# Kernel tuning notes

Measured on AMD Instinct MI355X. Metric: run time of the kernel, lower is better.

The kernel has to match this reference:

```python
import jax, jax.numpy as jnp
import numpy as np

NUM_EMBEDDINGS = 1024
EMBEDDING_DIM = 256
COMMITMENT_COST = 0.02


def setup_inputs() -> dict:
    key = jax.random.key(0)
    k1, k2 = jax.random.split(key)
    z = jax.random.normal(k1, (64, 256, 32, 32), dtype=jnp.float32)
    # torch init: uniform(-1/K, 1/K)
    emb = jax.random.uniform(k2, (NUM_EMBEDDINGS, EMBEDDING_DIM), dtype=jnp.float32,
                             minval=-1.0 / NUM_EMBEDDINGS, maxval=1.0 / NUM_EMBEDDINGS)
    return {"z": z, "emb": emb}


def reference(z, emb):
    n, d, h, w = z.shape
    # (N, D, H, W) -> (N*H*W, D)
    z_flat = jnp.transpose(z, (0, 2, 3, 1)).reshape(-1, d)
    # squared L2 distances: ||z||^2 - 2 z.E^T + ||E||^2  -> (NHW, K)
    distances = (jnp.sum(z_flat * z_flat, axis=1, keepdims=True)
                 - 2.0 * z_flat @ emb.T
                 + jnp.sum(emb * emb, axis=1))
    indices = jnp.argmin(distances, axis=1)  # (NHW,)
    z_q = jnp.transpose(emb[indices].reshape(n, h, w, d), (0, 3, 1, 2))  # (N, D, H, W)
    # straight-through estimator
    z_q_st = z + jax.lax.stop_gradient(z_q - z)
    commitment_loss = COMMITMENT_COST * jnp.mean((jax.lax.stop_gradient(z) - z_q) ** 2)
    codebook_loss = jnp.mean((z - jax.lax.stop_gradient(z_q)) ** 2)
    vq_loss = commitment_loss + codebook_loss
    indices_reshaped = indices.reshape(n, h, w)
    return z_q_st, indices_reshaped, vq_loss
```

## Files before the change

### kernel.cpp

```cpp
#include <hip/hip_runtime.h>
#include <hip/hip_bf16.h>
#include <float.h>

#define OUT_IDX_OFF 16777216
#define OUT_LOSS_OFF 16842752
#define CAND_OFF 8388608
#define GMIN_OFF 12582912
#define GCNT_OFF 13107200
#define NSLOT 32
#define DELTA 2.0e-3f

typedef __attribute__((ext_vector_type(8))) short short8;
typedef __attribute__((ext_vector_type(4))) float f32x4;

static __device__ __forceinline__ unsigned short f2bf(float f) {
  union { __hip_bfloat16 h; unsigned short u; } cv;
  cv.h = __float2bfloat16(f);
  return cv.u;
}

__global__ __launch_bounds__(256) void k_prep(const float* __restrict__ emb,
                                              unsigned short* __restrict__ E2,
                                              float* __restrict__ cws,
                                              int* __restrict__ gmin,
                                              int* __restrict__ gcnt,
                                              float* __restrict__ out) {
  const int k = blockIdx.x, d = threadIdx.x;
  const int tid = (k << 8) + d;
  if (tid < 65536) {
    gmin[tid] = 0x7f7f7f7f;
    gcnt[tid] = 0;
  }
  if (tid == 0) out[OUT_LOSS_OFF] = 0.0f;
  const float v = emb[k * 256 + d];
  __shared__ float red[256];
  __shared__ unsigned short row[256];
  row[d] = f2bf(v);
  red[d] = v * v;
  __syncthreads();
  for (int s = 128; s > 0; s >>= 1) {
    if (d < s) red[d] += red[d + s];
    __syncthreads();
  }
  if (d == 0) cws[k] = red[0];
  if (d < 32) ((short8*)&E2[k * 256])[d] = ((short8*)row)[d];
}

__global__ __launch_bounds__(256) void k_cvt4(const float* __restrict__ z,
                                              unsigned short* __restrict__ A2,
                                              float* __restrict__ aws) {
#pragma clang fp contract(off)
  __shared__ float tile[64][65];
  __shared__ float red2[128];
  const int t = threadIdx.x;
  const int p0 = blockIdx.x << 6;
  const int n = p0 >> 10, hw0 = p0 & 1023;
  const float* zb = z + (size_t)n * 262144 + hw0;
  const int hwl = (t & 15) << 2;
  const int dlb = t >> 4;
  const int row = t & 63, h = (t >> 6) & 1;
  const int pl = t >> 2, c = t & 3;

  float4 v[4];
#pragma unroll
  for (int i = 0; i < 4; ++i)
    v[i] = *(const float4*)&zb[(size_t)(dlb + i * 16) * 1024 + hwl];

  float acc[8];

  for (int dt = 0; dt < 4; ++dt) {
    if (dt) __syncthreads();
#pragma unroll
    for (int i = 0; i < 4; ++i) {
      const int dl = dlb + i * 16;
      tile[hwl + 0][dl] = v[i].x;
      tile[hwl + 1][dl] = v[i].y;
      tile[hwl + 2][dl] = v[i].z;
      tile[hwl + 3][dl] = v[i].w;
    }
    __syncthreads();
    if (dt < 3) {
      const float* zb2 = zb + (size_t)(dt + 1) * 65536;
#pragma unroll
      for (int i = 0; i < 4; ++i)
        v[i] = *(const float4*)&zb2[(size_t)(dlb + i * 16) * 1024 + hwl];
    }
    unsigned short* dst = &A2[(size_t)(p0 + pl) * 256 + dt * 64];
#pragma unroll
    for (int hh = 0; hh < 2; ++hh) {
      const int ch = c + hh * 4;
      unsigned short tmp[8];
#pragma unroll
      for (int j = 0; j < 8; ++j) tmp[j] = f2bf(tile[pl][ch * 8 + j]);
      *(short8*)&dst[ch * 8] = *(short8*)tmp;
    }
    if (t < 128 && (dt >> 1) == h) {
      if ((dt & 1) == 0) {
#pragma unroll
        for (int j = 0; j < 8; ++j) {
          const float x = tile[row][j];
          acc[j] = x * x;
        }
        for (int g = 1; g < 8; ++g)
#pragma unroll
          for (int j = 0; j < 8; ++j) {
            const float x = tile[row][g * 8 + j];
            const float p = x * x;
            acc[j] = acc[j] + p;
          }
      } else {
        for (int g = 8; g < 16; ++g)
#pragma unroll
          for (int j = 0; j < 8; ++j) {
            const float x = tile[row][(g - 8) * 8 + j];
            const float p = x * x;
            acc[j] = acc[j] + p;
          }
      }
    }
  }
  if (t < 128) {
    const float s = ((acc[0] + acc[1]) + (acc[2] + acc[3])) +
                    ((acc[4] + acc[5]) + (acc[6] + acc[7]));
    red2[t] = s;
  }
  __syncthreads();
  if (t < 64) aws[p0 + t] = red2[t] + red2[t + 64];
}

__global__ __launch_bounds__(256, 4) void k_gemm9(
    const unsigned short* __restrict__ A2, const unsigned short* __restrict__ E2,
    const float* __restrict__ cws, const float* __restrict__ aws,
    int* __restrict__ gmin, int* __restrict__ gcnt,
    float2* __restrict__ gcand) {
  __shared__ __align__(16) unsigned short As[128 * 64];
  __shared__ __align__(16) unsigned short Bs[128 * 64];
  __shared__ float a_l[128], c_l[128], rmkt[256], bmin[128];

  const int t = threadIdx.x;
  const int lane = t & 63;
  const int wave = __builtin_amdgcn_readfirstlane(t >> 6);
  const int wr = wave >> 1, wc = wave & 1;
  const int quad = lane >> 4, l15 = lane & 15;
  const int swa = l15 & 7;

  const int bid = blockIdx.x;
  const int L = ((bid & 7) << 9) + (bid >> 3);
  const int rb = L >> 3, ck = L & 7;
  const int r0 = rb << 7, k0 = ck << 7;

  if (t < 128) {
    a_l[t] = aws[r0 + t];
    c_l[t] = cws[k0 + t];
  }

  const int srow = t >> 3;
  const int gpos = t & 7;

  f32x4 acc[4][4];
#pragma unroll
  for (int a = 0; a < 4; ++a)
#pragma unroll
    for (int b = 0; b < 4; ++b) acc[a][b] = (f32x4)(0.0f);

  for (int kt = 0; kt < 4; ++kt) {
    if (kt) __syncthreads();
#pragma unroll
    for (int i = 0; i < 4; ++i) {
      const int row = (i << 5) + srow;
      const int gsrc = gpos ^ (row & 7);
      const unsigned short* sa =
          A2 + (((size_t)(r0 + row)) << 8) + (kt << 6) + (gsrc << 3);
      __builtin_amdgcn_global_load_lds(
          (const __attribute__((address_space(1))) void*)sa,
          (__attribute__((address_space(3))) void*)(As + (i << 11) +
                                                    (wave << 9)),
          16, 0, 0);
      const unsigned short* sb =
          E2 + (((size_t)(k0 + row)) << 8) + (kt << 6) + (gsrc << 3);
      __builtin_amdgcn_global_load_lds(
          (const __attribute__((address_space(1))) void*)sb,
          (__attribute__((address_space(3))) void*)(Bs + (i << 11) +
                                                    (wave << 9)),
          16, 0, 0);
    }
    __syncthreads();
#pragma unroll
    for (int ks = 0; ks < 2; ++ks) {
      short8 af[4], bf[4];
#pragma unroll
      for (int tr = 0; tr < 4; ++tr)
        af[tr] = *(const short8*)&As[(wr * 64 + tr * 16 + l15) * 64 +
                                     (((ks * 4 + quad) ^ swa) << 3)];
#pragma unroll
      for (int tc = 0; tc < 4; ++tc)
        bf[tc] = *(const short8*)&Bs[(wc * 64 + tc * 16 + l15) * 64 +
                                     (((ks * 4 + quad) ^ swa) << 3)];
#pragma unroll
      for (int tr = 0; tr < 4; ++tr)
#pragma unroll
        for (int tc = 0; tc < 4; ++tc)
          acc[tr][tc] = __builtin_amdgcn_mfma_f32_16x16x32_bf16(
              af[tr], bf[tc], acc[tr][tc], 0, 0, 0);
    }
  }

#pragma unroll
  for (int tr = 0; tr < 4; ++tr)
#pragma unroll
    for (int rg = 0; rg < 4; ++rg) {
      const int rloc = wr * 64 + tr * 16 + quad * 4 + rg;
      const float av = a_l[rloc];
      float mn = FLT_MAX;
#pragma unroll
      for (int tc = 0; tc < 4; ++tc) {
        const int cloc = wc * 64 + tc * 16 + l15;
        const float s = av + fmaf(-2.0f, acc[tr][tc][rg], c_l[cloc]);
        mn = fminf(mn, s);
      }
      mn = fminf(mn, __shfl_xor(mn, 1));
      mn = fminf(mn, __shfl_xor(mn, 2));
      mn = fminf(mn, __shfl_xor(mn, 4));
      mn = fminf(mn, __shfl_xor(mn, 8));
      if (l15 == 0) rmkt[rloc * 2 + wc] = mn;
    }
  __syncthreads();
  if (t < 128) {
    const float m = fminf(rmkt[t * 2], rmkt[t * 2 + 1]);
    const int old = atomicMin(&gmin[r0 + t], __float_as_int(m));
    bmin[t] = fminf(m, __int_as_float(old));
  }
  __syncthreads();
#pragma unroll
  for (int tr = 0; tr < 4; ++tr)
#pragma unroll
    for (int rg = 0; rg < 4; ++rg) {
      const int rloc = wr * 64 + tr * 16 + quad * 4 + rg;
      const float av = a_l[rloc];
      const float lim = bmin[rloc] + DELTA;
#pragma unroll
      for (int tc = 0; tc < 4; ++tc) {
        const int cloc = wc * 64 + tc * 16 + l15;
        const float s = av + fmaf(-2.0f, acc[tr][tc][rg], c_l[cloc]);
        if (s <= lim) {
          const int pos = atomicAdd(&gcnt[r0 + rloc], 1);
          if (pos < NSLOT)
            gcand[(size_t)(r0 + rloc) * NSLOT + pos] =
                make_float2(s, __int_as_float(k0 + cloc));
        }
      }
    }
}

__global__ __launch_bounds__(256) void k_finish6(
    const float* __restrict__ z, const float* __restrict__ emb,
    const float* __restrict__ cws, const float* __restrict__ aws,
    const int* __restrict__ gmin, const int* __restrict__ gcnt,
    const float2* __restrict__ gcand, int* __restrict__ idxws,
    float* __restrict__ out, int write_zq) {
  __shared__ float ztile[256][64];
  __shared__ int sidx[64];
  const int t = threadIdx.x;
  const int p0 = blockIdx.x << 6;
  const int n = p0 >> 10, hw0 = p0 & 1023;
  const float* zb = z + (size_t)n * 262144 + hw0;

  const int hwl = (t & 15) << 2;
  const int dl = t >> 4;
#pragma unroll
  for (int i = 0; i < 16; ++i) {
    const int d = dl + (i << 4);
    const float4 v = *(const float4*)&zb[(size_t)d * 1024 + hwl];
    ztile[d][hwl + 0] = v.x;
    ztile[d][hwl + 1] = v.y;
    ztile[d][hwl + 2] = v.z;
    ztile[d][hwl + 3] = v.w;
  }
  __syncthreads();

  const int pl = t >> 2, sub = t & 3;
  const int r = p0 + pl;
  const float lim = __int_as_float(gmin[r]) + DELTA;
  int m = gcnt[r];
  if (m > NSLOT) m = NSLOT;
  const float a = aws[r];
  float bestv = FLT_MAX;
  int besti = 0x7fffffff;
  for (int ci = sub; ci < m; ci += 4) {
    const float2 p = gcand[(size_t)r * NSLOT + ci];
    if (p.x > lim) continue;
    const int k = __float_as_int(p.y);
    const float4* ep4 = (const float4*)(emb + (size_t)k * 256);
    float dot = 0.0f;
#pragma unroll 16
    for (int j = 0; j < 64; ++j) {
      const float4 e = ep4[j];
      dot = fmaf(ztile[4 * j + 0][pl], e.x, dot);
      dot = fmaf(ztile[4 * j + 1][pl], e.y, dot);
      dot = fmaf(ztile[4 * j + 2][pl], e.z, dot);
      dot = fmaf(ztile[4 * j + 3][pl], e.w, dot);
    }
    float s = fmaf(-2.0f, dot, a);
    s = s + cws[k];
    if (s < bestv || (s == bestv && k < besti)) {
      bestv = s;
      besti = k;
    }
  }
#pragma unroll
  for (int off = 1; off < 4; off <<= 1) {
    const float ov = __shfl_xor(bestv, off);
    const int oi = __shfl_xor(besti, off);
    if (ov < bestv || (ov == bestv && oi < besti)) {
      bestv = ov;
      besti = oi;
    }
  }
  if (sub == 0) {
    out[OUT_IDX_OFF + r] = (float)besti;
    sidx[pl] = besti;
    if (!write_zq) idxws[r] = besti;
  }
  float c = (sub == 0) ? bestv : 0.0f;
#pragma unroll
  for (int off = 1; off < 64; off <<= 1) c += __shfl_xor(c, off);
  if ((t & 63) == 0)
    atomicAdd(&out[OUT_LOSS_OFF], c * (1.02f / 16777216.0f));

  if (write_zq) {
    __syncthreads();
    const int px = t & 63, dq = t >> 6;
    const float* ep = emb + (size_t)sidx[px] * 256 + (dq << 6);
    float* ob = out + (size_t)n * 262144 + ((size_t)(dq << 6)) * 1024 + hw0 + px;
#pragma unroll 8
    for (int i = 0; i < 64; ++i) ob[(size_t)i * 1024] = ep[i];
  }
}

__global__ __launch_bounds__(256) void k_out2(const float* __restrict__ emb,
                                              const int* __restrict__ idxws,
                                              float* __restrict__ out) {
  __shared__ float zq[32][257];
  __shared__ int sidx[32];
  const int t = threadIdx.x;
  const int p0 = blockIdx.x << 5;
  const int n = p0 >> 10, hw0 = p0 & 1023;
  if (t < 32) sidx[t] = idxws[p0 + t];
  __syncthreads();
#pragma unroll
  for (int it = 0; it < 8; ++it) {
    const int i = t + (it << 8);
    const int p = i >> 6;
    const int q = (i & 63) << 2;
    const float4 v = *(const float4*)&emb[(size_t)sidx[p] * 256 + q];
    zq[p][q] = v.x;
    zq[p][q + 1] = v.y;
    zq[p][q + 2] = v.z;
    zq[p][q + 3] = v.w;
  }
  __syncthreads();
  const int p = t & 31, d0 = t >> 5;
  float* ob = out + (size_t)n * 262144 + hw0 + p;
#pragma unroll
  for (int dd = 0; dd < 32; ++dd) {
    const int d = (dd << 3) + d0;
    ob[(size_t)d * 1024] = zq[p][d];
  }
}

extern "C" void kernel_launch(void* const* d_in, const int* in_sizes, int n_in,
                              void* d_out, int out_size, void* d_ws,
                              size_t ws_size, hipStream_t stream) {
  const float* z = (const float*)d_in[0];
  const float* emb = (const float*)d_in[1];
  float* out = (float*)d_out;

  unsigned short* E2 = (unsigned short*)d_ws;
  float* cws = (float*)(E2 + 262144);
  float* aws = cws + 1024;
  int* idxws = (int*)(aws + 65536);
  unsigned short* A2 = (unsigned short*)d_out;

  const size_t WS_NEED = 1052672u + 262144u + 262144u + 16777216u;
  const int big_ws = (ws_size >= WS_NEED) ? 1 : 0;
  int* gmin;
  int* gcnt;
  float2* gcand;
  if (big_ws) {
    gmin = idxws + 65536;
    gcnt = gmin + 65536;
    gcand = (float2*)(gcnt + 65536);
  } else {
    gcand = (float2*)(out + CAND_OFF);
    gmin = (int*)(out + GMIN_OFF);
    gcnt = (int*)(out + GCNT_OFF);
  }

  k_prep<<<dim3(1024), dim3(256), 0, stream>>>(emb, E2, cws, gmin, gcnt, out);
  k_cvt4<<<dim3(1024), dim3(256), 0, stream>>>(z, A2, aws);
  k_gemm9<<<dim3(4096), dim3(256), 0, stream>>>(A2, E2, cws, aws, gmin, gcnt,
                                                gcand);
  k_finish6<<<dim3(1024), dim3(256), 0, stream>>>(z, emb, cws, aws, gmin, gcnt,
                                                  gcand, idxws, out, big_ws);
  if (!big_ws)
    k_out2<<<dim3(2048), dim3(256), 0, stream>>>(emb, idxws, out);
}
```

Baseline: 290.0 us.

## Fuse prep/convert kernels and split GEMM tile across eight waves

Merges the codebook prep kernel and the z conversion kernel into one launch, using block-index ranges to pick the role. This removes one launch and lets the two independent jobs run side by side. The distance GEMM now runs 512 threads per block, with each wave computing a 32x64 sub-tile instead of 64x64. The aim is more waves for latency hiding and fewer accumulator registers per wave, at the cost of more LDS fragment reads per MFMA.

After: 289.7 us. No clear change (-0.1%).

```diff
diff --git a/kernel.cpp b/kernel.cpp
--- a/kernel.cpp
+++ b/kernel.cpp
@@ -19,41 +19,42 @@
   return cv.u;
 }
 
-__global__ __launch_bounds__(256) void k_prep(const float* __restrict__ emb,
-                                              unsigned short* __restrict__ E2,
-                                              float* __restrict__ cws,
-                                              int* __restrict__ gmin,
-                                              int* __restrict__ gcnt,
-                                              float* __restrict__ out) {
-  const int k = blockIdx.x, d = threadIdx.x;
-  const int tid = (k << 8) + d;
-  if (tid < 65536) {
-    gmin[tid] = 0x7f7f7f7f;
-    gcnt[tid] = 0;
-  }
-  if (tid == 0) out[OUT_LOSS_OFF] = 0.0f;
-  const float v = emb[k * 256 + d];
-  __shared__ float red[256];
-  __shared__ unsigned short row[256];
-  row[d] = f2bf(v);
-  red[d] = v * v;
-  __syncthreads();
-  for (int s = 128; s > 0; s >>= 1) {
-    if (d < s) red[d] += red[d + s];
+__global__ __launch_bounds__(256) void k_pc(
+    const float* __restrict__ z, const float* __restrict__ emb,
+    unsigned short* __restrict__ A2, float* __restrict__ aws,
+    unsigned short* __restrict__ E2, float* __restrict__ cws,
+    int* __restrict__ gmin, int* __restrict__ gcnt, float* __restrict__ out) {
+#pragma clang fp contract(off)
+  __shared__ __align__(16) float smem_f[64 * 65 + 128];
+  const int t = threadIdx.x;
+  const int bid = blockIdx.x;
+
+  if (bid >= 1024) {
+    const int k = bid - 1024, d = t;
+    float* red = smem_f;
+    unsigned short* row = (unsigned short*)(smem_f + 256);
+    const int tid = (k << 8) + d;
+    if (tid < 65536) {
+      gmin[tid] = 0x7f7f7f7f;
+      gcnt[tid] = 0;
+    }
+    if (tid == 0) out[OUT_LOSS_OFF] = 0.0f;
+    const float v = emb[k * 256 + d];
+    row[d] = f2bf(v);
+    red[d] = v * v;
     __syncthreads();
-  }
-  if (d == 0) cws[k] = red[0];
-  if (d < 32) ((short8*)&E2[k * 256])[d] = ((short8*)row)[d];
-}
-
-__global__ __launch_bounds__(256) void k_cvt4(const float* __restrict__ z,
-                                              unsigned short* __restrict__ A2,
-                                              float* __restrict__ aws) {
-#pragma clang fp contract(off)
-  __shared__ float tile[64][65];
-  __shared__ float red2[128];
-  const int t = threadIdx.x;
-  const int p0 = blockIdx.x << 6;
+    for (int s = 128; s > 0; s >>= 1) {
+      if (d < s) red[d] += red[d + s];
+      __syncthreads();
+    }
+    if (d == 0) cws[k] = red[0];
+    if (d < 32) ((short8*)&E2[k * 256])[d] = ((short8*)row)[d];
+    return;
+  }
+
+  float(*tile)[65] = (float(*)[65])smem_f;
+  float* red2 = smem_f + 64 * 65;
+  const int p0 = bid << 6;
   const int n = p0 >> 10, hw0 = p0 & 1023;
   const float* zb = z + (size_t)n * 262144 + hw0;
   const int hwl = (t & 15) << 2;
@@ -128,7 +129,7 @@
   if (t < 64) aws[p0 + t] = red2[t] + red2[t + 64];
 }
 
-__global__ __launch_bounds__(256, 4) void k_gemm9(
+__global__ __launch_bounds__(512, 6) void k_gemm11(
     const unsigned short* __restrict__ A2, const unsigned short* __restrict__ E2,
     const float* __restrict__ cws, const float* __restrict__ aws,
     int* __restrict__ gmin, int* __restrict__ gcnt,
@@ -157,47 +158,47 @@
   const int srow = t >> 3;
   const int gpos = t & 7;
 
-  f32x4 acc[4][4];
-#pragma unroll
-  for (int a = 0; a < 4; ++a)
+  f32x4 acc[2][4];
+#pragma unroll
+  for (int a = 0; a < 2; ++a)
 #pragma unroll
     for (int b = 0; b < 4; ++b) acc[a][b] = (f32x4)(0.0f);
 
   for (int kt = 0; kt < 4; ++kt) {
     if (kt) __syncthreads();
 #pragma unroll
-    for (int i = 0; i < 4; ++i) {
-      const int row = (i << 5) + srow;
+    for (int i = 0; i < 2; ++i) {
+      const int row = (i << 6) + srow;
       const int gsrc = gpos ^ (row & 7);
       const unsigned short* sa =
           A2 + (((size_t)(r0 + row)) << 8) + (kt << 6) + (gsrc << 3);
       __builtin_amdgcn_global_load_lds(
           (const __attribute__((address_space(1))) void*)sa,
-          (__attribute__((address_space(3))) void*)(As + (i << 11) +
+          (__attribute__((address_space(3))) void*)(As + (i << 12) +
                                                     (wave << 9)),
           16, 0, 0);
       const unsigned short* sb =
           E2 + (((size_t)(k0 + row)) << 8) + (kt << 6) + (gsrc << 3);
       __builtin_amdgcn_global_load_lds(
           (const __attribute__((address_space(1))) void*)sb,
-          (__attribute__((address_space(3))) void*)(Bs + (i << 11) +
+          (__attribute__((address_space(3))) void*)(Bs + (i << 12) +
                                                     (wave << 9)),
           16, 0, 0);
     }
     __syncthreads();
 #pragma unroll
     for (int ks = 0; ks < 2; ++ks) {
-      short8 af[4], bf[4];
-#pragma unroll
-      for (int tr = 0; tr < 4; ++tr)
-        af[tr] = *(const short8*)&As[(wr * 64 + tr * 16 + l15) * 64 +
+      short8 af[2], bf[4];
+#pragma unroll
+      for (int tr = 0; tr < 2; ++tr)
+        af[tr] = *(const short8*)&As[(wr * 32 + tr * 16 + l15) * 64 +
                                      (((ks * 4 + quad) ^ swa) << 3)];
 #pragma unroll
       for (int tc = 0; tc < 4; ++tc)
         bf[tc] = *(const short8*)&Bs[(wc * 64 + tc * 16 + l15) * 64 +
                                      (((ks * 4 + quad) ^ swa) << 3)];
 #pragma unroll
-      for (int tr = 0; tr < 4; ++tr)
+      for (int tr = 0; tr < 2; ++tr)
 #pragma unroll
         for (int tc = 0; tc < 4; ++tc)
           acc[tr][tc] = __builtin_amdgcn_mfma_f32_16x16x32_bf16(
@@ -206,10 +207,10 @@
   }
 
 #pragma unroll
-  for (int tr = 0; tr < 4; ++tr)
+  for (int tr = 0; tr < 2; ++tr)
 #pragma unroll
     for (int rg = 0; rg < 4; ++rg) {
-      const int rloc = wr * 64 + tr * 16 + quad * 4 + rg;
+      const int rloc = wr * 32 + tr * 16 + quad * 4 + rg;
       const float av = a_l[rloc];
       float mn = FLT_MAX;
 #pragma unroll
@@ -232,10 +233,10 @@
   }
   __syncthreads();
 #pragma unroll
-  for (int tr = 0; tr < 4; ++tr)
+  for (int tr = 0; tr < 2; ++tr)
 #pragma unroll
     for (int rg = 0; rg < 4; ++rg) {
-      const int rloc = wr * 64 + tr * 16 + quad * 4 + rg;
+      const int rloc = wr * 32 + tr * 16 + quad * 4 + rg;
       const float av = a_l[rloc];
       const float lim = bmin[rloc] + DELTA;
 #pragma unroll
@@ -396,10 +397,10 @@
     gcnt = (int*)(out + GCNT_OFF);
   }
 
-  k_prep<<<dim3(1024), dim3(256), 0, stream>>>(emb, E2, cws, gmin, gcnt, out);
-  k_cvt4<<<dim3(1024), dim3(256), 0, stream>>>(z, A2, aws);
-  k_gemm9<<<dim3(4096), dim3(256), 0, stream>>>(A2, E2, cws, aws, gmin, gcnt,
-                                                gcand);
+  k_pc<<<dim3(2048), dim3(256), 0, stream>>>(z, emb, A2, aws, E2, cws, gmin,
+                                             gcnt, out);
+  k_gemm11<<<dim3(4096), dim3(512), 0, stream>>>(A2, E2, cws, aws, gmin, gcnt,
+                                                 gcand);
   k_finish6<<<dim3(1024), dim3(256), 0, stream>>>(z, emb, cws, aws, gmin, gcnt,
                                                   gcand, idxws, out, big_ws);
   if (!big_ws)
```
